# Kernel tuning notes

Hardware: AMD Instinct MI355X
Metric: run time of the kernel (lower is better)

Reference implementation:

```python
import jax, jax.numpy as jnp
import numpy as np

N, B, H, L, FE = 32768, 256, 128, 4, 4
E = 262144


def setup_inputs() -> dict:
    key = jax.random.key(0)
    ks = jax.random.split(key, 16)
    def g(i, shape, scale=0.05):
        return jax.random.normal(ks[i], shape, dtype=jnp.float32) * scale
    return {
        "d": jax.random.uniform(ks[0], (E,), dtype=jnp.float32) * 5.0,
        "src": jax.random.randint(ks[1], (E,), 0, N),
        "dst": jax.random.randint(ks[2], (E,), 0, N),
        "seg": jnp.sort(jax.random.randint(ks[3], (N,), 0, B)),
        "node_emb": g(4, (H,), 1.0),
        "We": g(5, (2 * FE + 1, H)), "be": jnp.zeros((H,), jnp.float32),
        "msg_W1": g(6, (L, 3 * H, H)), "msg_b1": jnp.zeros((L, H), jnp.float32),
        "msg_W2": g(7, (L, H, H)), "msg_b2": jnp.zeros((L, H), jnp.float32),
        "soft_W": g(8, (L, H)), "soft_b": jnp.zeros((L,), jnp.float32),
        "upd_W1": g(9, (L, H, H)), "upd_b1": jnp.zeros((L, H), jnp.float32),
        "upd_W2": g(10, (L, H, H)), "upd_b2": jnp.zeros((L, H), jnp.float32),
        "out_W1": g(11, (H, H)), "out_b1": jnp.zeros((H,), jnp.float32),
        "out_W2": g(12, (H, H)), "out_b2": jnp.zeros((H,), jnp.float32),
    }


def reference(d, src, dst, seg, node_emb, We, be, msg_W1, msg_b1, msg_W2, msg_b2,
              soft_W, soft_b, upd_W1, upd_b1, upd_W2, upd_b2,
              out_W1, out_b1, out_W2, out_b2):
    silu = jax.nn.silu
    # fourier_encode_dist: [E] -> [E, 2*FE+1] = [sin(d/2^k), cos(d/2^k), d]
    scales = 2.0 ** jnp.arange(FE, dtype=d.dtype)
    x = d[:, None] / scales
    de = jnp.concatenate([jnp.sin(x), jnp.cos(x), d[:, None]], axis=-1)
    # edge_input MLP (1 layer, last_activation=SiLU) then extra F.silu in input_edge_func
    e = silu(silu(de @ We + be))                              # [E, H]
    # node_embedding broadcast to all nodes
    feat = jnp.broadcast_to(node_emb, (N, H))
    for l in range(L):
        mi = jnp.concatenate([feat[src], feat[dst], e], axis=-1)        # [E, 3H]
        m = silu(silu(mi @ msg_W1[l] + msg_b1[l]) @ msg_W2[l] + msg_b2[l])  # [E, H]
        e = e + m                                             # edge residual update
        w = jax.nn.sigmoid(m @ soft_W[l] + soft_b[l])[:, None]  # soft edge gate [E,1]
        msum = jax.ops.segment_sum(m * w, dst, num_segments=N)  # reduce to dst nodes
        upd_in = msum + feat
        feat = silu(upd_in @ upd_W1[l] + upd_b1[l]) @ upd_W2[l] + upd_b2[l] + feat
    # node-wise output network (2 layers, last activation None)
    feat = silu(feat @ out_W1 + out_b1) @ out_W2 + out_b2
    # multi-aggregator readout over graphs in batch
    s = jax.ops.segment_sum(feat, seg, num_segments=B)
    cnt = jax.ops.segment_sum(jnp.ones((N, 1), feat.dtype), seg, num_segments=B)
    mean = s / jnp.maximum(cnt, 1.0)
    mx = jax.ops.segment_max(feat, seg, num_segments=B)
    return jnp.concatenate([s, mean, mx], axis=-1)            # [B, 3H]
```

## Files before the change

kernel.cpp:

```cpp
#include <hip/hip_runtime.h>

#define NN 32768
#define NB 256
#define HD 128
#define NL 4
#define NE 262144

typedef short bf16x8 __attribute__((ext_vector_type(8)));
typedef float f32x4 __attribute__((ext_vector_type(4)));
typedef unsigned short u16;
typedef unsigned int u32;

__device__ __forceinline__ float bf2f(u16 u) {
  return __uint_as_float(((u32)u) << 16);
}
__device__ __forceinline__ u16 f2bf(float f) {
  u32 x = __float_as_uint(f);
  u32 r = x + 0x7FFFu + ((x >> 16) & 1u);
  return (u16)(r >> 16);
}
__device__ __forceinline__ u32 pk2(float a, float b) {
  return (u32)f2bf(a) | ((u32)f2bf(b) << 16);
}
__device__ __forceinline__ float siluf(float x) {
  return x * __builtin_amdgcn_rcpf(1.0f + __expf(-x));
}
__device__ __forceinline__ float sigf(float x) {
  return __builtin_amdgcn_rcpf(1.0f + __expf(-x));
}
__device__ __forceinline__ u32 ordu(float f) {
  u32 b = __float_as_uint(f);
  return (b & 0x80000000u) ? ~b : (b | 0x80000000u);
}

__device__ __forceinline__ float ldinf(const void* p, size_t i, int mode) {
  return mode ? ((const float*)p)[i] : bf2f(((const u16*)p)[i]);
}
__device__ __forceinline__ u16 ldinb(const void* p, size_t i, int mode) {
  return mode ? f2bf(((const float*)p)[i]) : ((const u16*)p)[i];
}

__global__ void k_detect(const u16* __restrict__ Weraw, int* __restrict__ flag) {
  if (threadIdx.x == 0 && blockIdx.x == 0) {
    int cnt = 0;
    for (int i = 0; i < 256; i++) {
      u16 u = Weraw[2 * i];
      u32 e = (u >> 7) & 0xFFu;
      if (e >= 112u && e <= 126u) cnt++;
    }
    *flag = (cnt >= 128) ? 0 : 1;
  }
}


__global__ __launch_bounds__(256) void k_csr_deg(const int* __restrict__ dstp,
                                                 u32* __restrict__ deg) {
  const int i = blockIdx.x * 256 + threadIdx.x;
  atomicAdd(&deg[dstp[i]], 1u);
}

__global__ __launch_bounds__(1024) void k_csr_scan(const u32* __restrict__ deg,
                                                   int* __restrict__ rowptr,
                                                   int* __restrict__ cursor) {
  __shared__ int part[1024];
  const int t = threadIdx.x;
  int loc[32];
  int s = 0;
#pragma unroll
  for (int j = 0; j < 32; j++) { loc[j] = s; s += (int)deg[t * 32 + j]; }
  part[t] = s;
  __syncthreads();
  int inc = s;
  for (int off = 1; off < 1024; off <<= 1) {
    int tmp = (t >= off) ? part[t - off] : 0;
    __syncthreads();
    part[t] += tmp;
    __syncthreads();
  }
  const int base = part[t] - inc;
#pragma unroll
  for (int j = 0; j < 32; j++) {
    rowptr[t * 32 + j] = base + loc[j];
    cursor[t * 32 + j] = base + loc[j];
  }
  if (t == 1023) rowptr[NN] = part[1023];
}

__global__ __launch_bounds__(256) void k_csr_scatter(const int* __restrict__ dstp,
                                                     const int* __restrict__ srcp,
                                                     int* __restrict__ cursor,
                                                     int* __restrict__ eids,
                                                     int* __restrict__ src_s,
                                                     int* __restrict__ dst_s) {
  const int i = blockIdx.x * 256 + threadIdx.x;
  const int d = dstp[i];
  const int pos = atomicAdd(&cursor[d], 1);
  eids[pos] = i;
  src_s[pos] = srcp[i];
  dst_s[pos] = d;
}

#define PANEL 16384

template <int MT>
__device__ __forceinline__ void acc_zero(f32x4 (&acc)[MT][8]) {
#pragma unroll
  for (int mt = 0; mt < MT; mt++)
#pragma unroll
    for (int nt = 0; nt < 8; nt++) acc[mt][nt] = f32x4{0.f, 0.f, 0.f, 0.f};
}

template <int MT>
__device__ __forceinline__ void gemm_gp(const u16* __restrict__ A0,
                                        const size_t* rowoff,
                                        const u16* __restrict__ Bp,
                                        int l, int kg, f32x4 (&acc)[MT][8]) {
#pragma unroll
  for (int ks = 0; ks < 4; ks++) {
    bf16x8 a[MT];
#pragma unroll
    for (int mt = 0; mt < MT; mt++)
      a[mt] = *(const bf16x8*)&A0[rowoff[mt] + ks * 32 + kg * 8];
#pragma unroll
    for (int nt = 0; nt < 8; nt++) {
      bf16x8 b = *(const bf16x8*)&Bp[(size_t)((nt * 4 + ks) * 64 + l) * 8];
#pragma unroll
      for (int mt = 0; mt < MT; mt++)
        acc[mt][nt] = __builtin_amdgcn_mfma_f32_16x16x32_bf16(a[mt], b, acc[mt][nt], 0, 0, 0);
    }
  }
}

template <int MT>
__device__ __forceinline__ void wave_gemm_p(const short* lAw, const u16* __restrict__ Bp,
                                            int l, int c, int kg, f32x4 (&acc)[MT][8]) {
#pragma unroll
  for (int ks = 0; ks < 4; ks++) {
    bf16x8 a[MT];
#pragma unroll
    for (int mt = 0; mt < MT; mt++) {
      const int r = mt * 16 + c;
      const int k = ks * 32 + kg * 8;
      a[mt] = *(const bf16x8*)&lAw[r * HD + (k ^ ((r & 7) << 3))];
    }
#pragma unroll
    for (int nt = 0; nt < 8; nt++) {
      bf16x8 b = *(const bf16x8*)&Bp[(size_t)((nt * 4 + ks) * 64 + l) * 8];
#pragma unroll
      for (int mt = 0; mt < MT; mt++)
        acc[mt][nt] = __builtin_amdgcn_mfma_f32_16x16x32_bf16(a[mt], b, acc[mt][nt], 0, 0, 0);
    }
  }
}

template <int MT, bool SILU>
__device__ __forceinline__ void wave_pack(short* lAw, int c, int kg,
                                          f32x4 (&acc)[MT][8], const float* bias) {
#pragma unroll
  for (int mt = 0; mt < MT; mt++) {
#pragma unroll
    for (int rr = 0; rr < 4; rr++) {
      const int row = mt * 16 + kg * 4 + rr;
      u32 ou[4];
#pragma unroll
      for (int p = 0; p < 4; p++) {
        float x0 = acc[mt][2 * p][rr] + bias[2 * p];
        float x1 = acc[mt][2 * p + 1][rr] + bias[2 * p + 1];
        if (SILU) { x0 = siluf(x0); x1 = siluf(x1); }
        ou[p] = pk2(x0, x1);
      }
      ((int4*)(lAw + row * HD))[c ^ (row & 7)] =
          make_int4((int)ou[0], (int)ou[1], (int)ou[2], (int)ou[3]);
    }
  }
}

__global__ __launch_bounds__(256) void k_prep(
    const void* __restrict__ mW1, const void* __restrict__ mW2,
    const void* __restrict__ uW1, const void* __restrict__ uW2,
    const void* __restrict__ oW1, const void* __restrict__ oW2,
    const int* __restrict__ flagp,
    u16* __restrict__ Wt1, u16* __restrict__ Wt2p,
    u16* __restrict__ Wtu1, u16* __restrict__ Wtu2p,
    u16* __restrict__ Wto1, u16* __restrict__ Wto2p) {
  const int mode = *flagp;
  const int tid = blockIdx.x * blockDim.x + threadIdx.x;
  const int stride = gridDim.x * blockDim.x;
  for (int i = tid; i < NL * 3 * PANEL; i += stride) {
    const int l = i / (3 * PANEL), r = i % (3 * PANEL);
    const int chunk = r / PANEL, r2 = r % PANEL;
    const int nt = r2 / 2048, ks = (r2 % 2048) / 512;
    const int lane = (r2 % 512) / 8, j = r2 % 8;
    const int s = ks * 32 + (lane >> 4) * 8 + j;
    const int klog = ((s & 7) << 4) | (s >> 3);
    const int n = nt * 16 + (lane & 15);
    Wt1[i] = ldinb(mW1, ((size_t)l * 384 + chunk * 128 + klog) * HD + n, mode);
  }
  for (int i = tid; i < NL * PANEL; i += stride) {
    const int l = i / PANEL, r = i % PANEL;
    const int nt = r / 2048, ks = (r % 2048) / 512;
    const int lane = (r % 512) / 8, j = r % 8;
    const int s = ks * 32 + (lane >> 4) * 8 + j;
    const int klog = ((s & 7) << 4) | (s >> 3);
    const int n = nt * 16 + (lane & 15);
    Wt2p[i] = ldinb(mW2, ((size_t)l * HD + klog) * HD + n, mode);
    Wtu1[i] = ldinb(uW1, ((size_t)l * HD + klog) * HD + n, mode);
    Wtu2p[i] = ldinb(uW2, ((size_t)l * HD + klog) * HD + n, mode);
  }
  for (int i = tid; i < PANEL; i += stride) {
    const int nt = i / 2048, ks = (i % 2048) / 512;
    const int lane = (i % 512) / 8, j = i % 8;
    const int s = ks * 32 + (lane >> 4) * 8 + j;
    const int klog = ((s & 7) << 4) | (s >> 3);
    const int n = nt * 16 + (lane & 15);
    Wto1[i] = ldinb(oW1, (size_t)klog * HD + n, mode);
    Wto2p[i] = ldinb(oW2, (size_t)klog * HD + n, mode);
  }
}

__global__ __launch_bounds__(256) void k_featinit(const void* __restrict__ nemb,
                                                  const int* __restrict__ flagp,
                                                  u16* __restrict__ feat) {
  const int mode = *flagp;
  const int i = blockIdx.x * 256 + threadIdx.x;
  const int g = i & 15;
  u32 ou[4];
#pragma unroll
  for (int p = 0; p < 4; p++) {
    u16 a = ldinb(nemb, (2 * p) * 16 + g, mode);
    u16 b = ldinb(nemb, (2 * p + 1) * 16 + g, mode);
    ou[p] = (u32)a | ((u32)b << 16);
  }
  ((int4*)feat)[i] = make_int4((int)ou[0], (int)ou[1], (int)ou[2], (int)ou[3]);
}

__global__ __launch_bounds__(256) void k_encode(const void* __restrict__ d,
                                                const int* __restrict__ eids,
                                                const void* __restrict__ We,
                                                const void* __restrict__ be,
                                                const int* __restrict__ flagp,
                                                u16* __restrict__ e) {
  const int mode = *flagp;
  __shared__ float sW[9 * HD];
  __shared__ float sb[HD];
  for (int i = threadIdx.x; i < 9 * HD; i += 256) sW[i] = ldinf(We, i, mode);
  for (int i = threadIdx.x; i < HD; i += 256) sb[i] = ldinf(be, i, mode);
  __syncthreads();
  const int spos = blockIdx.x * 256 + threadIdx.x;
  const float dv = ldinf(d, eids[spos], mode);
  float de[9];
#pragma unroll
  for (int k = 0; k < 4; k++) {
    float x = dv * (1.0f / (float)(1 << k));
    de[k] = __sinf(x);
    de[4 + k] = __cosf(x);
  }
  de[8] = dv;
  u16* erow = e + (size_t)spos * HD;
#pragma unroll
  for (int g = 0; g < 16; g++) {
    u32 ou[4];
#pragma unroll
    for (int p = 0; p < 4; p++) {
      float vv[2];
#pragma unroll
      for (int t = 0; t < 2; t++) {
        const int h = (2 * p + t) * 16 + g;
        float a = sb[h];
#pragma unroll
        for (int k = 0; k < 9; k++) a += de[k] * sW[k * HD + h];
        vv[t] = siluf(siluf(a));
      }
      ou[p] = pk2(vv[0], vv[1]);
    }
    ((int4*)erow)[g] = make_int4((int)ou[0], (int)ou[1], (int)ou[2], (int)ou[3]);
  }
}

__global__ __launch_bounds__(64, 4) void k_edge(
    const u16* __restrict__ feat, u16* __restrict__ e,
    const int* __restrict__ src_s, const int* __restrict__ dst_s,
    const u16* __restrict__ Wt1, const u16* __restrict__ Wt2p,
    const void* __restrict__ b1g, const void* __restrict__ b2g,
    const void* __restrict__ softW, const void* __restrict__ softb,
    const int* __restrict__ flagp, float* __restrict__ msum, int layer) {
  __shared__ __align__(16) short lM[32 * HD];
  __shared__ float swg[32];
  __shared__ int sdst[32];
  const int mode = *flagp;
  const int l = threadIdx.x;
  const int c = l & 15, kg = l >> 4;
  const int blk = blockIdx.x * 32;

  if (l < 32) sdst[l] = dst_s[blk + l];

  size_t offS[2], offD[2], offE[2];
#pragma unroll
  for (int mt = 0; mt < 2; mt++) {
    const int eidx = blk + mt * 16 + c;
    offS[mt] = (size_t)src_s[eidx] * HD;
    offD[mt] = (size_t)dst_s[eidx] * HD;
    offE[mt] = (size_t)eidx * HD;
  }

  const u16* W1l = Wt1 + (size_t)layer * 3 * PANEL;
  const u16* W2l = Wt2p + (size_t)layer * PANEL;
  float bias1[8], bias2[8], swf[8];
#pragma unroll
  for (int nt = 0; nt < 8; nt++) {
    bias1[nt] = ldinf(b1g, layer * HD + nt * 16 + c, mode);
    bias2[nt] = ldinf(b2g, layer * HD + nt * 16 + c, mode);
    swf[nt] = ldinf(softW, (size_t)layer * HD + nt * 16 + c, mode);
  }
  const float sbv = ldinf(softb, layer, mode);

  f32x4 acc[2][8];
  acc_zero<2>(acc);
  gemm_gp<2>(feat, offS, W1l, l, kg, acc);
  gemm_gp<2>(feat, offD, W1l + PANEL, l, kg, acc);
  gemm_gp<2>(e, offE, W1l + 2 * PANEL, l, kg, acc);
  wave_pack<2, true>(lM, c, kg, acc, bias1);
  __syncthreads();

  acc_zero<2>(acc);
  wave_gemm_p<2>(lM, W2l, l, c, kg, acc);
  __syncthreads();

  float wred[2][4];
#pragma unroll
  for (int mt = 0; mt < 2; mt++) {
#pragma unroll
    for (int rr = 0; rr < 4; rr++) {
      const int row = mt * 16 + kg * 4 + rr;
      float mv[8];
      float wp = 0.f;
#pragma unroll
      for (int nt = 0; nt < 8; nt++) {
        mv[nt] = siluf(acc[mt][nt][rr] + bias2[nt]);
        wp += mv[nt] * swf[nt];
      }
      u32 ou[4];
#pragma unroll
      for (int p = 0; p < 4; p++) ou[p] = pk2(mv[2 * p], mv[2 * p + 1]);
      ((int4*)(lM + row * HD))[c ^ (row & 7)] =
          make_int4((int)ou[0], (int)ou[1], (int)ou[2], (int)ou[3]);
      wp += __shfl_xor(wp, 1);
      wp += __shfl_xor(wp, 2);
      wp += __shfl_xor(wp, 4);
      wp += __shfl_xor(wp, 8);
      wred[mt][rr] = wp;
    }
  }
#pragma unroll
  for (int mt = 0; mt < 2; mt++)
#pragma unroll
    for (int rr = 0; rr < 4; rr++)
      if (c == mt * 4 + rr) swg[mt * 16 + kg * 4 + rr] = sigf(wred[mt][rr] + sbv);
  __syncthreads();

  const int gL = l >> 2;
  const int eoff = (l & 3) * 2;
  const int gM = ((l >> 3) << 3);
  const int em = l & 7;
  float a0 = 0.f, a1 = 0.f;
  int cur = sdst[0];
  for (int r = 0; r < 32; r++) {
    const int dn = sdst[r];
    if (dn != cur) {
      atomicAdd(&msum[(size_t)cur * HD + l], a0);
      atomicAdd(&msum[(size_t)cur * HD + l + 64], a1);
      a0 = 0.f; a1 = 0.f; cur = dn;
    }
    const int rx = (r & 7) << 3;
    const float wgr = swg[r];
    a0 += wgr * bf2f((u16)lM[r * HD + (gM ^ rx) + em]);
    a1 += wgr * bf2f((u16)lM[r * HD + (gM ^ rx) + 64 + em]);
    const u32 mv = *(const u32*)&lM[r * HD + ((gL ^ (r & 7)) << 3) + eoff];
    u32* erow32 = (u32*)(e + (size_t)(blk + r) * HD);
    const u32 old = erow32[l];
    erow32[l] = pk2(bf2f((u16)(old & 0xffffu)) + bf2f((u16)(mv & 0xffffu)),
                    bf2f((u16)(old >> 16)) + bf2f((u16)(mv >> 16)));
  }
  atomicAdd(&msum[(size_t)cur * HD + l], a0);
  atomicAdd(&msum[(size_t)cur * HD + l + 64], a1);
}

__global__ __launch_bounds__(64, 2) void k_node(
    u16* __restrict__ feat, const float* __restrict__ msum,
    const u16* __restrict__ Wtu1, const u16* __restrict__ Wtu2p,
    const void* __restrict__ b1g, const void* __restrict__ b2g,
    const int* __restrict__ flagp, int layer) {
  __shared__ __align__(16) short lA[64 * HD];
  const int mode = *flagp;
  const int l = threadIdx.x;
  const int c = l & 15, kg = l >> 4;
  short* lAw = lA;
  const int blkn = blockIdx.x * 64;
  const int myrow = blkn + l;
  u16* frow = feat + (size_t)myrow * HD;
  const float* mrow = msum + (size_t)myrow * HD;
  const u16* W1l = Wtu1 + (size_t)layer * PANEL;
  const u16* W2l = Wtu2p + (size_t)layer * PANEL;
  float bias1[8], bias2[8];
#pragma unroll
  for (int nt = 0; nt < 8; nt++) {
    bias1[nt] = ldinf(b1g, layer * HD + nt * 16 + c, mode);
    bias2[nt] = ldinf(b2g, layer * HD + nt * 16 + c, mode);
  }
  {
    int4* lrow = (int4*)(lAw + l * HD);
#pragma unroll
    for (int g = 0; g < 16; g++) {
      int4 fv = ((const int4*)frow)[g];
      u32 uu[4] = {(u32)fv.x, (u32)fv.y, (u32)fv.z, (u32)fv.w};
      float4 ma = ((const float4*)mrow)[2 * g];
      float4 mb = ((const float4*)mrow)[2 * g + 1];
      float mm[8] = {ma.x, ma.y, ma.z, ma.w, mb.x, mb.y, mb.z, mb.w};
      u32 ou[4];
#pragma unroll
      for (int p = 0; p < 4; p++) {
        float a0 = bf2f((u16)(uu[p] & 0xffffu)) + mm[2 * p];
        float a1 = bf2f((u16)(uu[p] >> 16)) + mm[2 * p + 1];
        ou[p] = pk2(a0, a1);
      }
      lrow[g ^ (l & 7)] = make_int4((int)ou[0], (int)ou[1], (int)ou[2], (int)ou[3]);
    }
  }
  __syncthreads();
  f32x4 acc[4][8];
  acc_zero<4>(acc);
  wave_gemm_p<4>(lAw, W1l, l, c, kg, acc);
  __syncthreads();
  wave_pack<4, true>(lAw, c, kg, acc, bias1);
  __syncthreads();
  acc_zero<4>(acc);
  wave_gemm_p<4>(lAw, W2l, l, c, kg, acc);
  __syncthreads();
  wave_pack<4, false>(lAw, c, kg, acc, bias2);
  __syncthreads();

  const int gL = l >> 2;
  const int eoff = (l & 3) * 2;
#pragma unroll 4
  for (int r = 0; r < 64; r++) {
    const u32 mv = *(const u32*)&lAw[r * HD + ((gL ^ (r & 7)) << 3) + eoff];
    u32* frow32 = (u32*)(feat + (size_t)(blkn + r) * HD);
    const u32 old = frow32[l];
    frow32[l] = pk2(bf2f((u16)(old & 0xffffu)) + bf2f((u16)(mv & 0xffffu)),
                    bf2f((u16)(old >> 16)) + bf2f((u16)(mv >> 16)));
  }
}

__global__ __launch_bounds__(64, 2) void k_out(
    const u16* __restrict__ feat, const int* __restrict__ seg,
    const u16* __restrict__ Wto1, const u16* __restrict__ Wto2p,
    const void* __restrict__ ob1, const void* __restrict__ ob2,
    const int* __restrict__ flagp,
    float* __restrict__ sacc, u32* __restrict__ mxacc, float* __restrict__ cnt) {
  __shared__ __align__(16) short lA[64 * HD];
  __shared__ int sseg[64];
  const int mode = *flagp;
  const int l = threadIdx.x;
  const int c = l & 15, kg = l >> 4;
  short* lAw = lA;
  const int myrow = blockIdx.x * 64 + l;
  const u16* frow = feat + (size_t)myrow * HD;
  float bias1[8], bias2[8];
#pragma unroll
  for (int nt = 0; nt < 8; nt++) {
    bias1[nt] = ldinf(ob1, nt * 16 + c, mode);
    bias2[nt] = ldinf(ob2, nt * 16 + c, mode);
  }
  {
    int4* lrow = (int4*)(lAw + l * HD);
#pragma unroll
    for (int g = 0; g < 16; g++) lrow[g ^ (l & 7)] = ((const int4*)frow)[g];
  }
  sseg[l] = seg[myrow];
  __syncthreads();
  f32x4 acc[4][8];
  acc_zero<4>(acc);
  wave_gemm_p<4>(lAw, Wto1, l, c, kg, acc);
  __syncthreads();
  wave_pack<4, true>(lAw, c, kg, acc, bias1);
  __syncthreads();
  acc_zero<4>(acc);
  wave_gemm_p<4>(lAw, Wto2p, l, c, kg, acc);
  __syncthreads();
  wave_pack<4, false>(lAw, c, kg, acc, bias2);
  __syncthreads();

  const int gL = l >> 2;
  const int eoff = (l & 3) * 2;
  const bool uniform = (sseg[0] == sseg[63]);
  if (uniform) {
    const int g = sseg[0];
    float s1 = 0.f, s2 = 0.f, x1 = -3.402823e38f, x2 = -3.402823e38f;
#pragma unroll 4
    for (int r = 0; r < 64; r++) {
      const u32 mv = *(const u32*)&lAw[r * HD + ((gL ^ (r & 7)) << 3) + eoff];
      const float v1 = bf2f((u16)(mv & 0xffffu));
      const float v2 = bf2f((u16)(mv >> 16));
      s1 += v1; s2 += v2;
      x1 = fmaxf(x1, v1); x2 = fmaxf(x2, v2);
    }
    atomicAdd(&sacc[(size_t)g * HD + 2 * l], s1);
    atomicAdd(&sacc[(size_t)g * HD + 2 * l + 1], s2);
    atomicMax(&mxacc[(size_t)g * HD + 2 * l], ordu(x1));
    atomicMax(&mxacc[(size_t)g * HD + 2 * l + 1], ordu(x2));
    if (l == 0) atomicAdd(&cnt[g], 64.0f);
  } else {
    atomicAdd(&cnt[sseg[l]], 1.0f);
#pragma unroll 4
    for (int r = 0; r < 64; r++) {
      const u32 mv = *(const u32*)&lAw[r * HD + ((gL ^ (r & 7)) << 3) + eoff];
      const float v1 = bf2f((u16)(mv & 0xffffu));
      const float v2 = bf2f((u16)(mv >> 16));
      const int g = sseg[r];
      atomicAdd(&sacc[(size_t)g * HD + 2 * l], v1);
      atomicAdd(&sacc[(size_t)g * HD + 2 * l + 1], v2);
      atomicMax(&mxacc[(size_t)g * HD + 2 * l], ordu(v1));
      atomicMax(&mxacc[(size_t)g * HD + 2 * l + 1], ordu(v2));
    }
  }
}

__global__ __launch_bounds__(256) void k_final(const float* __restrict__ sacc,
                                               const u32* __restrict__ mxacc,
                                               const float* __restrict__ cnt,
                                               const int* __restrict__ flagp,
                                               void* __restrict__ out) {
  const int mode = *flagp;
  const int i = blockIdx.x * 256 + threadIdx.x;
  const int b = i / 384, j = i % 384;
  float v;
  if (j < HD) {
    const int p = ((j & 15) << 3) | (j >> 4);
    v = sacc[b * HD + p];
  } else if (j < 2 * HD) {
    const int t = j - HD;
    const int p = ((t & 15) << 3) | (t >> 4);
    v = sacc[b * HD + p] / fmaxf(cnt[b], 1.0f);
  } else {
    const int t = j - 2 * HD;
    const int p = ((t & 15) << 3) | (t >> 4);
    u32 u = mxacc[b * HD + p];
    u32 bits = (u >> 31) ? (u ^ 0x80000000u) : ~u;
    v = __uint_as_float(bits);
  }
  if (mode) ((float*)out)[i] = v;
  else ((u16*)out)[i] = f2bf(v);
}

extern "C" void kernel_launch(void* const* d_in, const int* in_sizes, int n_in,
                              void* d_out, int out_size, void* d_ws, size_t ws_size,
                              hipStream_t stream) {
  const void* d_d = d_in[0];
  const int* src = (const int*)d_in[1];
  const int* dst = (const int*)d_in[2];
  const int* seg = (const int*)d_in[3];
  const void* nemb = d_in[4];
  const void* We = d_in[5];
  const void* be = d_in[6];
  const void* mW1 = d_in[7];
  const void* mb1 = d_in[8];
  const void* mW2 = d_in[9];
  const void* mb2 = d_in[10];
  const void* sW = d_in[11];
  const void* sb = d_in[12];
  const void* uW1 = d_in[13];
  const void* ub1 = d_in[14];
  const void* uW2 = d_in[15];
  const void* ub2 = d_in[16];
  const void* oW1 = d_in[17];
  const void* ob1 = d_in[18];
  const void* oW2 = d_in[19];
  const void* ob2 = d_in[20];

  char* ws = (char*)d_ws;
  const size_t OFF_E = 0;
  const size_t OFF_MSUM = OFF_E + (size_t)NE * HD * 2;
  const size_t OFF_FEAT = OFF_MSUM + (size_t)NN * HD * 4;
  const size_t OFF_SACC = OFF_FEAT + (size_t)NN * HD * 2;
  const size_t OFF_MX = OFF_SACC + (size_t)NB * HD * 4;
  const size_t OFF_CNT = OFF_MX + (size_t)NB * HD * 4;
  const size_t OFF_DEG = OFF_CNT + 1024;
  const size_t OFF_ROWPTR = OFF_DEG + (size_t)NN * 4;
  const size_t OFF_CURSOR = OFF_ROWPTR + (size_t)(NN + 2) * 4;
  const size_t OFF_EIDS = OFF_CURSOR + (size_t)NN * 4;
  const size_t OFF_SRCS = OFF_EIDS + (size_t)NE * 4;
  const size_t OFF_DSTS = OFF_SRCS + (size_t)NE * 4;
  const size_t OFF_WT1 = OFF_DSTS + (size_t)NE * 4;
  const size_t OFF_WT2P = OFF_WT1 + (size_t)NL * 3 * PANEL * 2;
  const size_t OFF_WTU1 = OFF_WT2P + (size_t)NL * PANEL * 2;
  const size_t OFF_WTU2P = OFF_WTU1 + (size_t)NL * PANEL * 2;
  const size_t OFF_WTO1 = OFF_WTU2P + (size_t)NL * PANEL * 2;
  const size_t OFF_WTO2P = OFF_WTO1 + (size_t)PANEL * 2;
  const size_t OFF_FLAG = OFF_WTO2P + (size_t)PANEL * 2;

  u16* e = (u16*)(ws + OFF_E);
  float* msum = (float*)(ws + OFF_MSUM);
  u16* feat = (u16*)(ws + OFF_FEAT);
  float* sacc = (float*)(ws + OFF_SACC);
  u32* mx = (u32*)(ws + OFF_MX);
  float* cnt = (float*)(ws + OFF_CNT);
  u32* deg = (u32*)(ws + OFF_DEG);
  int* rowptr = (int*)(ws + OFF_ROWPTR);
  int* cursor = (int*)(ws + OFF_CURSOR);
  int* eids = (int*)(ws + OFF_EIDS);
  int* src_s = (int*)(ws + OFF_SRCS);
  int* dst_s = (int*)(ws + OFF_DSTS);
  u16* Wt1 = (u16*)(ws + OFF_WT1);
  u16* Wt2p = (u16*)(ws + OFF_WT2P);
  u16* Wtu1 = (u16*)(ws + OFF_WTU1);
  u16* Wtu2p = (u16*)(ws + OFF_WTU2P);
  u16* Wto1 = (u16*)(ws + OFF_WTO1);
  u16* Wto2p = (u16*)(ws + OFF_WTO2P);
  int* flag = (int*)(ws + OFF_FLAG);

  hipMemsetAsync(ws + OFF_SACC, 0,
                 (size_t)NB * HD * 4 * 2 + 1024 + (size_t)NN * 4, stream);

  k_detect<<<1, 64, 0, stream>>>((const u16*)We, flag);
  k_prep<<<256, 256, 0, stream>>>(mW1, mW2, uW1, uW2, oW1, oW2, flag,
                                  Wt1, Wt2p, Wtu1, Wtu2p, Wto1, Wto2p);
  k_featinit<<<(NN * HD / 8) / 256, 256, 0, stream>>>(nemb, flag, feat);

  k_csr_deg<<<NE / 256, 256, 0, stream>>>(dst, deg);
  k_csr_scan<<<1, 1024, 0, stream>>>(deg, rowptr, cursor);
  k_csr_scatter<<<NE / 256, 256, 0, stream>>>(dst, src, cursor, eids, src_s, dst_s);

  k_encode<<<NE / 256, 256, 0, stream>>>(d_d, eids, We, be, flag, e);

  for (int l = 0; l < NL; l++) {
    hipMemsetAsync(msum, 0, (size_t)NN * HD * 4, stream);
    k_edge<<<NE / 32, 64, 0, stream>>>(feat, e, src_s, dst_s, Wt1, Wt2p,
                                       mb1, mb2, sW, sb, flag, msum, l);
    k_node<<<NN / 64, 64, 0, stream>>>(feat, msum, Wtu1, Wtu2p, ub1, ub2, flag, l);
  }
  k_out<<<NN / 64, 64, 0, stream>>>(feat, seg, Wto1, Wto2p, ob1, ob2, flag, sacc, mx, cnt);
  k_final<<<(NB * 384) / 256, 256, 0, stream>>>(sacc, mx, cnt, flag, d_out);
}
```

Measured before the change: 819.7 us.

## Fuse residual updates into GEMM epilogues, halve node tiles, use hardware bf16 pack

The edge kernel now adds the message to the edge residual directly from accumulator registers with int4 row accesses, instead of staging through LDS and doing a 32-bit-per-lane loop afterward. The node kernel likewise applies the feature residual straight from the second GEMM's accumulators. Node and output kernels move to 32-row tiles with coalesced row loads and a higher occupancy hint, launching twice as many blocks. The bf16 pair packing switches to the HIP intrinsic conversion, which may use native conversion instructions but could differ subtly in NaN handling.

```diff
diff --git a/kernel.cpp b/kernel.cpp
--- a/kernel.cpp
+++ b/kernel.cpp
@@ -1,4 +1,5 @@
 #include <hip/hip_runtime.h>
+#include <hip/hip_bf16.h>
 
 #define NN 32768
 #define NB 256
@@ -20,7 +21,8 @@
   return (u16)(r >> 16);
 }
 __device__ __forceinline__ u32 pk2(float a, float b) {
-  return (u32)f2bf(a) | ((u32)f2bf(b) << 16);
+  __hip_bfloat162 h = __float22bfloat162_rn(make_float2(a, b));
+  return *reinterpret_cast<u32*>(&h);
 }
 __device__ __forceinline__ float siluf(float x) {
   return x * __builtin_amdgcn_rcpf(1.0f + __expf(-x));
@@ -332,6 +334,9 @@
 #pragma unroll
     for (int rr = 0; rr < 4; rr++) {
       const int row = mt * 16 + kg * 4 + rr;
+      int4* erow4 = (int4*)(e + (size_t)(blk + row) * HD);
+      const int4 eo = erow4[c];
+      const u32 eu[4] = {(u32)eo.x, (u32)eo.y, (u32)eo.z, (u32)eo.w};
       float mv[8];
       float wp = 0.f;
 #pragma unroll
@@ -339,11 +344,16 @@
         mv[nt] = siluf(acc[mt][nt][rr] + bias2[nt]);
         wp += mv[nt] * swf[nt];
       }
-      u32 ou[4];
-#pragma unroll
-      for (int p = 0; p < 4; p++) ou[p] = pk2(mv[2 * p], mv[2 * p + 1]);
+      u32 mo[4], ou[4];
+#pragma unroll
+      for (int p = 0; p < 4; p++) {
+        mo[p] = pk2(mv[2 * p], mv[2 * p + 1]);
+        ou[p] = pk2(bf2f((u16)(eu[p] & 0xffffu)) + mv[2 * p],
+                    bf2f((u16)(eu[p] >> 16)) + mv[2 * p + 1]);
+      }
       ((int4*)(lM + row * HD))[c ^ (row & 7)] =
-          make_int4((int)ou[0], (int)ou[1], (int)ou[2], (int)ou[3]);
+          make_int4((int)mo[0], (int)mo[1], (int)mo[2], (int)mo[3]);
+      erow4[c] = make_int4((int)ou[0], (int)ou[1], (int)ou[2], (int)ou[3]);
       wp += __shfl_xor(wp, 1);
       wp += __shfl_xor(wp, 2);
       wp += __shfl_xor(wp, 4);
@@ -358,8 +368,6 @@
       if (c == mt * 4 + rr) swg[mt * 16 + kg * 4 + rr] = sigf(wred[mt][rr] + sbv);
   __syncthreads();
 
-  const int gL = l >> 2;
-  const int eoff = (l & 3) * 2;
   const int gM = ((l >> 3) << 3);
   const int em = l & 7;
   float a0 = 0.f, a1 = 0.f;
@@ -375,30 +383,22 @@
     const float wgr = swg[r];
     a0 += wgr * bf2f((u16)lM[r * HD + (gM ^ rx) + em]);
     a1 += wgr * bf2f((u16)lM[r * HD + (gM ^ rx) + 64 + em]);
-    const u32 mv = *(const u32*)&lM[r * HD + ((gL ^ (r & 7)) << 3) + eoff];
-    u32* erow32 = (u32*)(e + (size_t)(blk + r) * HD);
-    const u32 old = erow32[l];
-    erow32[l] = pk2(bf2f((u16)(old & 0xffffu)) + bf2f((u16)(mv & 0xffffu)),
-                    bf2f((u16)(old >> 16)) + bf2f((u16)(mv >> 16)));
   }
   atomicAdd(&msum[(size_t)cur * HD + l], a0);
   atomicAdd(&msum[(size_t)cur * HD + l + 64], a1);
 }
 
-__global__ __launch_bounds__(64, 2) void k_node(
+__global__ __launch_bounds__(64, 4) void k_node(
     u16* __restrict__ feat, const float* __restrict__ msum,
     const u16* __restrict__ Wtu1, const u16* __restrict__ Wtu2p,
     const void* __restrict__ b1g, const void* __restrict__ b2g,
     const int* __restrict__ flagp, int layer) {
-  __shared__ __align__(16) short lA[64 * HD];
+  __shared__ __align__(16) short lA[32 * HD];
   const int mode = *flagp;
   const int l = threadIdx.x;
   const int c = l & 15, kg = l >> 4;
   short* lAw = lA;
-  const int blkn = blockIdx.x * 64;
-  const int myrow = blkn + l;
-  u16* frow = feat + (size_t)myrow * HD;
-  const float* mrow = msum + (size_t)myrow * HD;
+  const int blkn = blockIdx.x * 32;
   const u16* W1l = Wtu1 + (size_t)layer * PANEL;
   const u16* W2l = Wtu2p + (size_t)layer * PANEL;
   float bias1[8], bias2[8];
@@ -407,97 +407,103 @@
     bias1[nt] = ldinf(b1g, layer * HD + nt * 16 + c, mode);
     bias2[nt] = ldinf(b2g, layer * HD + nt * 16 + c, mode);
   }
-  {
-    int4* lrow = (int4*)(lAw + l * HD);
-#pragma unroll
-    for (int g = 0; g < 16; g++) {
-      int4 fv = ((const int4*)frow)[g];
-      u32 uu[4] = {(u32)fv.x, (u32)fv.y, (u32)fv.z, (u32)fv.w};
-      float4 ma = ((const float4*)mrow)[2 * g];
-      float4 mb = ((const float4*)mrow)[2 * g + 1];
-      float mm[8] = {ma.x, ma.y, ma.z, ma.w, mb.x, mb.y, mb.z, mb.w};
+#pragma unroll
+  for (int rp = 0; rp < 8; rp++) {
+    const int r = rp * 4 + (l >> 4);
+    const int g = l & 15;
+    const int4 fv = ((const int4*)(feat + (size_t)(blkn + r) * HD))[g];
+    const u32 uu[4] = {(u32)fv.x, (u32)fv.y, (u32)fv.z, (u32)fv.w};
+    const float4 ma = ((const float4*)(msum + (size_t)(blkn + r) * HD))[2 * g];
+    const float4 mb = ((const float4*)(msum + (size_t)(blkn + r) * HD))[2 * g + 1];
+    const float mm[8] = {ma.x, ma.y, ma.z, ma.w, mb.x, mb.y, mb.z, mb.w};
+    u32 ou[4];
+#pragma unroll
+    for (int p = 0; p < 4; p++) {
+      ou[p] = pk2(bf2f((u16)(uu[p] & 0xffffu)) + mm[2 * p],
+                  bf2f((u16)(uu[p] >> 16)) + mm[2 * p + 1]);
+    }
+    ((int4*)(lAw + r * HD))[g ^ (r & 7)] =
+        make_int4((int)ou[0], (int)ou[1], (int)ou[2], (int)ou[3]);
+  }
+  __syncthreads();
+  f32x4 acc[2][8];
+  acc_zero<2>(acc);
+  wave_gemm_p<2>(lAw, W1l, l, c, kg, acc);
+  __syncthreads();
+  wave_pack<2, true>(lAw, c, kg, acc, bias1);
+  __syncthreads();
+  acc_zero<2>(acc);
+  wave_gemm_p<2>(lAw, W2l, l, c, kg, acc);
+
+#pragma unroll
+  for (int mt = 0; mt < 2; mt++) {
+#pragma unroll
+    for (int rr = 0; rr < 4; rr++) {
+      const int row = mt * 16 + kg * 4 + rr;
+      int4* frow4 = (int4*)(feat + (size_t)(blkn + row) * HD);
+      const int4 fo = frow4[c];
+      const u32 fu[4] = {(u32)fo.x, (u32)fo.y, (u32)fo.z, (u32)fo.w};
       u32 ou[4];
 #pragma unroll
       for (int p = 0; p < 4; p++) {
-        float a0 = bf2f((u16)(uu[p] & 0xffffu)) + mm[2 * p];
-        float a1 = bf2f((u16)(uu[p] >> 16)) + mm[2 * p + 1];
-        ou[p] = pk2(a0, a1);
+        const float x0 = acc[mt][2 * p][rr] + bias2[2 * p];
+        const float x1 = acc[mt][2 * p + 1][rr] + bias2[2 * p + 1];
+        ou[p] = pk2(bf2f((u16)(fu[p] & 0xffffu)) + x0,
+                    bf2f((u16)(fu[p] >> 16)) + x1);
       }
-      lrow[g ^ (l & 7)] = make_int4((int)ou[0], (int)ou[1], (int)ou[2], (int)ou[3]);
-    }
-  }
-  __syncthreads();
-  f32x4 acc[4][8];
-  acc_zero<4>(acc);
-  wave_gemm_p<4>(lAw, W1l, l, c, kg, acc);
-  __syncthreads();
-  wave_pack<4, true>(lAw, c, kg, acc, bias1);
-  __syncthreads();
-  acc_zero<4>(acc);
-  wave_gemm_p<4>(lAw, W2l, l, c, kg, acc);
-  __syncthreads();
-  wave_pack<4, false>(lAw, c, kg, acc, bias2);
-  __syncthreads();
-
-  const int gL = l >> 2;
-  const int eoff = (l & 3) * 2;
-#pragma unroll 4
-  for (int r = 0; r < 64; r++) {
-    const u32 mv = *(const u32*)&lAw[r * HD + ((gL ^ (r & 7)) << 3) + eoff];
-    u32* frow32 = (u32*)(feat + (size_t)(blkn + r) * HD);
-    const u32 old = frow32[l];
-    frow32[l] = pk2(bf2f((u16)(old & 0xffffu)) + bf2f((u16)(mv & 0xffffu)),
-                    bf2f((u16)(old >> 16)) + bf2f((u16)(mv >> 16)));
-  }
-}
-
-__global__ __launch_bounds__(64, 2) void k_out(
+      frow4[c] = make_int4((int)ou[0], (int)ou[1], (int)ou[2], (int)ou[3]);
+    }
+  }
+}
+
+__global__ __launch_bounds__(64, 4) void k_out(
     const u16* __restrict__ feat, const int* __restrict__ seg,
     const u16* __restrict__ Wto1, const u16* __restrict__ Wto2p,
     const void* __restrict__ ob1, const void* __restrict__ ob2,
     const int* __restrict__ flagp,
     float* __restrict__ sacc, u32* __restrict__ mxacc, float* __restrict__ cnt) {
-  __shared__ __align__(16) short lA[64 * HD];
-  __shared__ int sseg[64];
+  __shared__ __align__(16) short lA[32 * HD];
+  __shared__ int sseg[32];
   const int mode = *flagp;
   const int l = threadIdx.x;
   const int c = l & 15, kg = l >> 4;
   short* lAw = lA;
-  const int myrow = blockIdx.x * 64 + l;
-  const u16* frow = feat + (size_t)myrow * HD;
+  const int blkn = blockIdx.x * 32;
   float bias1[8], bias2[8];
 #pragma unroll
   for (int nt = 0; nt < 8; nt++) {
     bias1[nt] = ldinf(ob1, nt * 16 + c, mode);
     bias2[nt] = ldinf(ob2, nt * 16 + c, mode);
   }
-  {
-    int4* lrow = (int4*)(lAw + l * HD);
-#pragma unroll
-    for (int g = 0; g < 16; g++) lrow[g ^ (l & 7)] = ((const int4*)frow)[g];
-  }
-  sseg[l] = seg[myrow];
-  __syncthreads();
-  f32x4 acc[4][8];
-  acc_zero<4>(acc);
-  wave_gemm_p<4>(lAw, Wto1, l, c, kg, acc);
-  __syncthreads();
-  wave_pack<4, true>(lAw, c, kg, acc, bias1);
-  __syncthreads();
-  acc_zero<4>(acc);
-  wave_gemm_p<4>(lAw, Wto2p, l, c, kg, acc);
-  __syncthreads();
-  wave_pack<4, false>(lAw, c, kg, acc, bias2);
+#pragma unroll
+  for (int rp = 0; rp < 8; rp++) {
+    const int r = rp * 4 + (l >> 4);
+    const int g = l & 15;
+    ((int4*)(lAw + r * HD))[g ^ (r & 7)] =
+        ((const int4*)(feat + (size_t)(blkn + r) * HD))[g];
+  }
+  if (l < 32) sseg[l] = seg[blkn + l];
+  __syncthreads();
+  f32x4 acc[2][8];
+  acc_zero<2>(acc);
+  wave_gemm_p<2>(lAw, Wto1, l, c, kg, acc);
+  __syncthreads();
+  wave_pack<2, true>(lAw, c, kg, acc, bias1);
+  __syncthreads();
+  acc_zero<2>(acc);
+  wave_gemm_p<2>(lAw, Wto2p, l, c, kg, acc);
+  __syncthreads();
+  wave_pack<2, false>(lAw, c, kg, acc, bias2);
   __syncthreads();
 
   const int gL = l >> 2;
   const int eoff = (l & 3) * 2;
-  const bool uniform = (sseg[0] == sseg[63]);
+  const bool uniform = (sseg[0] == sseg[31]);
   if (uniform) {
     const int g = sseg[0];
     float s1 = 0.f, s2 = 0.f, x1 = -3.402823e38f, x2 = -3.402823e38f;
 #pragma unroll 4
-    for (int r = 0; r < 64; r++) {
+    for (int r = 0; r < 32; r++) {
       const u32 mv = *(const u32*)&lAw[r * HD + ((gL ^ (r & 7)) << 3) + eoff];
       const float v1 = bf2f((u16)(mv & 0xffffu));
       const float v2 = bf2f((u16)(mv >> 16));
@@ -508,11 +514,11 @@
     atomicAdd(&sacc[(size_t)g * HD + 2 * l + 1], s2);
     atomicMax(&mxacc[(size_t)g * HD + 2 * l], ordu(x1));
     atomicMax(&mxacc[(size_t)g * HD + 2 * l + 1], ordu(x2));
-    if (l == 0) atomicAdd(&cnt[g], 64.0f);
+    if (l == 0) atomicAdd(&cnt[g], 32.0f);
   } else {
-    atomicAdd(&cnt[sseg[l]], 1.0f);
+    if (l < 32) atomicAdd(&cnt[sseg[l]], 1.0f);
 #pragma unroll 4
-    for (int r = 0; r < 64; r++) {
+    for (int r = 0; r < 32; r++) {
       const u32 mv = *(const u32*)&lAw[r * HD + ((gL ^ (r & 7)) << 3) + eoff];
       const float v1 = bf2f((u16)(mv & 0xffffu));
       const float v2 = bf2f((u16)(mv >> 16));
@@ -636,8 +642,8 @@
     hipMemsetAsync(msum, 0, (size_t)NN * HD * 4, stream);
     k_edge<<<NE / 32, 64, 0, stream>>>(feat, e, src_s, dst_s, Wt1, Wt2p,
                                        mb1, mb2, sW, sb, flag, msum, l);
-    k_node<<<NN / 64, 64, 0, stream>>>(feat, msum, Wtu1, Wtu2p, ub1, ub2, flag, l);
-  }
-  k_out<<<NN / 64, 64, 0, stream>>>(feat, seg, Wto1, Wto2p, ob1, ob2, flag, sacc, mx, cnt);
+    k_node<<<NN / 32, 64, 0, stream>>>(feat, msum, Wtu1, Wtu2p, ub1, ub2, flag, l);
+  }
+  k_out<<<NN / 32, 64, 0, stream>>>(feat, seg, Wto1, Wto2p, ob1, ob2, flag, sacc, mx, cnt);
   k_final<<<(NB * 384) / 256, 256, 0, stream>>>(sacc, mx, cnt, flag, d_out);
 }
```

Measured after the change: 763.2 us. -6.9%, faster.
